# Performance work log

Measured on AMD Instinct MI355X. Metric: run time of the kernel, lower is better.

## Reference

```python
import jax, jax.numpy as jnp
import numpy as np

H = 8          # num_heads
EPS = 1e-5     # LayerNorm eps (torch default)


def _layernorm(x, gamma, beta):
    mu = jnp.mean(x, axis=-1, keepdims=True)
    var = jnp.mean(jnp.square(x - mu), axis=-1, keepdims=True)
    return (x - mu) * jax.lax.rsqrt(var + EPS) * gamma + beta


def setup_inputs() -> dict:
    key = jax.random.key(0)
    ks = jax.random.split(key, 20)
    B, S, D, F = 32, 1024, 256, 512
    d = D // H
    s = 1.0 / np.sqrt(D)
    sf = 1.0 / np.sqrt(F)
    inp = {
        "x": jax.random.normal(ks[0], (B, S, D), jnp.float32),
        "hidden": jax.random.normal(ks[1], (B, H, S, d), jnp.float32),
        # attention projections (torch Linear layout: [out, in])
        "Wq": jax.random.uniform(ks[2], (D, D), jnp.float32, -s, s),
        "bq": jnp.zeros((D,), jnp.float32),
        "Wk": jax.random.uniform(ks[3], (D, D), jnp.float32, -s, s),
        "bk": jnp.zeros((D,), jnp.float32),
        "Wv": jax.random.uniform(ks[4], (D, D), jnp.float32, -s, s),
        "bv": jnp.zeros((D,), jnp.float32),
        "Wo": jax.random.uniform(ks[5], (D, D), jnp.float32, -s, s),
        "bo": jnp.zeros((D,), jnp.float32),
        # layernorms
        "g1": jnp.ones((D,), jnp.float32),
        "be1": jnp.zeros((D,), jnp.float32),
        "g2": jnp.ones((D,), jnp.float32),
        "be2": jnp.zeros((D,), jnp.float32),
        # feed-forward
        "W1": jax.random.uniform(ks[6], (F, D), jnp.float32, -s, s),
        "b1": jnp.zeros((F,), jnp.float32),
        "W2": jax.random.uniform(ks[7], (D, F), jnp.float32, -sf, sf),
        "b2": jnp.zeros((D,), jnp.float32),
    }
    return inp


def reference(x, hidden, Wq, bq, Wk, bk, Wv, bv, Wo, bo, g1, be1, g2, be2, W1, b1, W2, b2):
    B, S, D = x.shape
    d = D // H
    scale = 1.0 / np.sqrt(d)

    def split_heads(t):  # [B,S,D] -> [B,H,S,d]
        return t.reshape(B, S, H, d).transpose(0, 2, 1, 3)

    q = split_heads(x @ Wq.T + bq)
    k = split_heads(x @ Wk.T + bk)
    v = split_heads(x @ Wv.T + bv)

    # scores with extra hidden-dependent bias: (q k^T + hidden k^T) / sqrt(d)
    scores = jnp.einsum("bhqd,bhkd->bhqk", q, k) * scale
    scores = scores + jnp.einsum("bhqd,bhkd->bhqk", hidden, k) * scale
    attn = jax.nn.softmax(scores, axis=-1)                 # [B,H,S,S]

    ctx = jnp.einsum("bhqk,bhkd->bhqd", attn, v)           # [B,H,S,d]
    ctx = ctx.transpose(0, 2, 1, 3).reshape(B, S, D)
    attn_out = ctx @ Wo.T + bo

    # x = x + x  (note: residual input discarded, attention output doubled)
    h = attn_out + attn_out
    # FFN with residual (dropout is identity at inference)
    h_norm = _layernorm(h, g1, be1)
    ff = jax.nn.relu(h_norm @ W1.T + b1) @ W2.T + b2
    h = h + ff
    # final: x = x + LayerNorm(x)
    h = h + _layernorm(h, g2, be2)
    return (h, attn)
```

## Files before the change

### kernel.cpp

```cpp
#include <hip/hip_runtime.h>

typedef __attribute__((ext_vector_type(8))) short short8;
typedef __attribute__((ext_vector_type(4))) float f32x4;

constexpr int NB  = 32;
constexpr int NS  = 1024;
constexpr int ND  = 256;
constexpr int NH  = 8;
constexpr int NDH = 32;
constexpr int NF  = 512;
constexpr int NM  = NB * NS;
#define RSD 0.17677669529663687f

static __device__ __forceinline__ ushort f2bf(float f) {
    union { float f; unsigned u; } v; v.f = f;
    unsigned r = v.u + 0x7fffu + ((v.u >> 16) & 1u);
    return (ushort)(r >> 16);
}
static __device__ __forceinline__ float bf2f(ushort u) {
    union { unsigned u; float f; } v; v.u = (unsigned)u << 16; return v.f;
}

__global__ __launch_bounds__(256) void split_hi(
    const float* __restrict__ in, ushort* __restrict__ hi, int n4)
{
    int i = blockIdx.x * 256 + threadIdx.x;
    if (i >= n4) return;
    float4 v = ((const float4*)in)[i];
    ushort4 h;
    h.x = f2bf(v.x); h.y = f2bf(v.y); h.z = f2bf(v.z); h.w = f2bf(v.w);
    ((ushort4*)hi)[i] = h;
}

__global__ __launch_bounds__(256) void split_weights(
    const float* __restrict__ Wq, const float* __restrict__ Wk,
    const float* __restrict__ Wv, const float* __restrict__ Wo,
    const float* __restrict__ W1, const float* __restrict__ W2,
    ushort* __restrict__ whi, ushort* __restrict__ wlo)
{
    const int seg = blockIdx.y;
    const float* src;
    size_t off;
    int n4;
    switch (seg) {
        case 0: src = Wq; off = 0;      n4 = 16384; break;
        case 1: src = Wk; off = 65536;  n4 = 16384; break;
        case 2: src = Wv; off = 131072; n4 = 16384; break;
        case 3: src = Wo; off = 196608; n4 = 16384; break;
        case 4: src = W1; off = 262144; n4 = 32768; break;
        default: src = W2; off = 393216; n4 = 32768; break;
    }
    int i = blockIdx.x * 256 + threadIdx.x;
    if (i >= n4) return;
    float4 v = ((const float4*)src)[i];
    ushort4 h, l;
    h.x = f2bf(v.x); l.x = f2bf(v.x - bf2f(h.x));
    h.y = f2bf(v.y); l.y = f2bf(v.y - bf2f(h.y));
    h.z = f2bf(v.z); l.z = f2bf(v.z - bf2f(h.z));
    h.w = f2bf(v.w); l.w = f2bf(v.w - bf2f(h.w));
    ((ushort4*)(whi + off))[i] = h;
    ((ushort4*)(wlo + off))[i] = l;
}

#define GEMM_CORE(K_, TERMS_)                                                  \
    __shared__ ushort sAh[128 * 40];                                           \
    __shared__ ushort sAl[(TERMS_ == 3) ? 128 * 40 : 8];                       \
    __shared__ ushort sBh[128 * 40], sBl[128 * 40];                            \
    const int t = threadIdx.x;                                                 \
    const int w = t >> 6, ln = t & 63;                                         \
    const int wr = w >> 1, wc = w & 1;                                         \
    const int col = ln & 15, quad = ln >> 4;                                   \
    const int srow = t >> 1, skb = (t & 1) << 4;                               \
    const ushort* gAh = Ahi + (size_t)(rbase + srow) * (K_) + skb;             \
    const ushort* gAl = (TERMS_ == 3) ? Alo + (size_t)(rbase + srow) * (K_) + skb : gAh; \
    const ushort* gBh = Whi + (size_t)(jbase + srow) * (K_) + skb;             \
    const ushort* gBl = Wlo + (size_t)(jbase + srow) * (K_) + skb;             \
    ushort* wAh = &sAh[srow * 40 + skb];                                       \
    ushort* wAl = (TERMS_ == 3) ? &sAl[srow * 40 + skb] : wAh;                 \
    ushort* wBh = &sBh[srow * 40 + skb];                                       \
    ushort* wBl = &sBl[srow * 40 + skb];                                       \
    f32x4 acc[4][4] = {};                                                      \
    short8 a0 = *(const short8*)(gAh);                                         \
    short8 a1 = *(const short8*)(gAh + 8);                                     \
    short8 c0 = {}, c1 = {};                                                   \
    if (TERMS_ == 3) { c0 = *(const short8*)(gAl); c1 = *(const short8*)(gAl + 8); } \
    short8 b0 = *(const short8*)(gBh);                                         \
    short8 b1 = *(const short8*)(gBh + 8);                                     \
    short8 d0 = *(const short8*)(gBl);                                         \
    short8 d1 = *(const short8*)(gBl + 8);                                     \
    for (int k0 = 0; k0 < (K_); k0 += 32) {                                    \
        __syncthreads();                                                       \
        *(short8*)wAh = a0; *(short8*)(wAh + 8) = a1;                          \
        if (TERMS_ == 3) { *(short8*)wAl = c0; *(short8*)(wAl + 8) = c1; }     \
        *(short8*)wBh = b0; *(short8*)(wBh + 8) = b1;                          \
        *(short8*)wBl = d0; *(short8*)(wBl + 8) = d1;                          \
        __syncthreads();                                                       \
        if (k0 + 32 < (K_)) {                                                  \
            a0 = *(const short8*)(gAh + k0 + 32);                              \
            a1 = *(const short8*)(gAh + k0 + 40);                              \
            if (TERMS_ == 3) {                                                 \
                c0 = *(const short8*)(gAl + k0 + 32);                          \
                c1 = *(const short8*)(gAl + k0 + 40);                          \
            }                                                                  \
            b0 = *(const short8*)(gBh + k0 + 32);                              \
            b1 = *(const short8*)(gBh + k0 + 40);                              \
            d0 = *(const short8*)(gBl + k0 + 32);                              \
            d1 = *(const short8*)(gBl + k0 + 40);                              \
        }                                                                      \
        short8 af[4], afl[4], bfv[4], bfl[4];                                  \
        _Pragma("unroll")                                                      \
        for (int m = 0; m < 4; ++m) {                                          \
            af[m]  = *(const short8*)&sAh[(wr * 64 + m * 16 + col) * 40 + quad * 8]; \
            if (TERMS_ == 3)                                                   \
                afl[m] = *(const short8*)&sAl[(wr * 64 + m * 16 + col) * 40 + quad * 8]; \
            bfv[m] = *(const short8*)&sBh[(wc * 64 + m * 16 + col) * 40 + quad * 8]; \
            bfl[m] = *(const short8*)&sBl[(wc * 64 + m * 16 + col) * 40 + quad * 8]; \
        }                                                                      \
        _Pragma("unroll")                                                      \
        for (int m = 0; m < 4; ++m)                                            \
            _Pragma("unroll")                                                  \
            for (int n = 0; n < 4; ++n) {                                      \
                acc[m][n] = __builtin_amdgcn_mfma_f32_16x16x32_bf16(af[m],  bfv[n], acc[m][n], 0, 0, 0); \
                acc[m][n] = __builtin_amdgcn_mfma_f32_16x16x32_bf16(af[m],  bfl[n], acc[m][n], 0, 0, 0); \
                if (TERMS_ == 3)                                               \
                    acc[m][n] = __builtin_amdgcn_mfma_f32_16x16x32_bf16(afl[m], bfv[n], acc[m][n], 0, 0, 0); \
            }                                                                  \
    }

template<int TERMS>
__global__ __launch_bounds__(256, TERMS == 2 ? 3 : 2) void gemm_mfma(
    const ushort* __restrict__ Ahi, const ushort* __restrict__ Alo,
    const ushort* __restrict__ Whi, const ushort* __restrict__ Wlo,
    const float* __restrict__ bias,
    float* __restrict__ outf, ushort* __restrict__ ohi,
    int N, int K, int epi)
{
    const int rbase = blockIdx.y << 7;
    const int jbase = blockIdx.x << 7;
    GEMM_CORE(K, TERMS)

    #pragma unroll
    for (int n = 0; n < 4; ++n) {
        const int cg = jbase + wc * 64 + n * 16 + col;
        const float bs = bias[cg];
        #pragma unroll
        for (int m = 0; m < 4; ++m) {
            #pragma unroll
            for (int r = 0; r < 4; ++r) {
                const int row = rbase + wr * 64 + m * 16 + quad * 4 + r;
                float v = acc[m][n][r] + bs;
                size_t oidx = (size_t)row * N + cg;
                if (epi == 0) {
                    outf[oidx] = 2.f * v;
                } else if (epi == 1) {
                    ohi[oidx] = f2bf(fmaxf(v, 0.f));
                } else {
                    outf[oidx] += v;
                }
            }
        }
    }
}

__global__ __launch_bounds__(256, 3) void gemm_qkv_mfma(
    const ushort* __restrict__ xhi,
    const ushort* __restrict__ whi, const ushort* __restrict__ wlo,
    const float* __restrict__ bq, const float* __restrict__ bk, const float* __restrict__ bv,
    const float* __restrict__ hidden,
    ushort* __restrict__ qhi, ushort* __restrict__ qlo,
    ushort* __restrict__ khi, ushort* __restrict__ klo,
    float* __restrict__ vb)
{
    const int z = blockIdx.z;
    const int rbase = blockIdx.y << 7;
    const int jbase = blockIdx.x << 7;
    const ushort* Ahi = xhi;
    const ushort* Alo = xhi;
    const ushort* Whi = whi + (size_t)z * 65536;
    const ushort* Wlo = wlo + (size_t)z * 65536;
    const float* bias = (z == 0) ? bq : (z == 1) ? bk : bv;
    GEMM_CORE(ND, 2)

    #pragma unroll
    for (int n = 0; n < 4; ++n) {
        const int cg = jbase + wc * 64 + n * 16 + col;
        const float bs = bias[cg];
        const int hh = cg >> 5, dd = cg & 31;
        #pragma unroll
        for (int m = 0; m < 4; ++m) {
            #pragma unroll
            for (int r = 0; r < 4; ++r) {
                const int row = rbase + wr * 64 + m * 16 + quad * 4 + r;
                const int b_i = row >> 10, s_i = row & 1023;
                size_t idx = (((size_t)(b_i * NH + hh)) * NS + s_i) * NDH + dd;
                float v = acc[m][n][r] + bs;
                if (z == 2) {
                    vb[idx] = v;
                } else if (z == 0) {
                    v = (v + hidden[idx]) * RSD;
                    ushort h = f2bf(v);
                    qhi[idx] = h;
                    qlo[idx] = f2bf(v - bf2f(h));
                } else {
                    ushort h = f2bf(v);
                    khi[idx] = h;
                    klo[idx] = f2bf(v - bf2f(h));
                }
            }
        }
    }
}

constexpr int VS  = 136;
constexpr int PST = 136;
__global__ __launch_bounds__(256, 4) void attn_flash(
    const ushort* __restrict__ qhi, const ushort* __restrict__ qlo,
    const ushort* __restrict__ khi, const ushort* __restrict__ klo,
    const float* __restrict__ vb,
    float* __restrict__ attn, ushort* __restrict__ cthi, ushort* __restrict__ ctlo)
{
    __shared__ ushort Vthi[32 * VS];
    __shared__ ushort Vtlo[32 * VS];
    __shared__ ushort Ps[4][16 * PST];
    const int bid = blockIdx.x;
    const int lid = (bid & 7) * 512 + (bid >> 3);
    const int qt = lid & 15, bh = lid >> 4;
    const int q0 = qt << 6;
    const int t = threadIdx.x;
    const int w = t >> 6, ln = t & 63;
    const int col = ln & 15, quad = ln >> 4;
    const int qr0 = q0 + 16 * w;
    ushort* myP = Ps[w];

    const size_t bhbase = (size_t)bh * NS * NDH;
    const size_t aoff = bhbase + (size_t)(qr0 + col) * NDH + quad * 8;
    const short8 ahi = *(const short8*)(qhi + aoff);
    const short8 alo = *(const short8*)(qlo + aoff);

    const float* vbase = vb + bhbase;
    const int sdd = t & 31, skg = (t >> 5) << 4;

    f32x4 acc0 = {0.f, 0.f, 0.f, 0.f}, acc1 = {0.f, 0.f, 0.f, 0.f};
    float S[4] = {0.f, 0.f, 0.f, 0.f};

    for (int k0 = 0; k0 < NS; k0 += 128) {
        __syncthreads();
        ushort hs[16], ls[16];
        #pragma unroll
        for (int c = 0; c < 16; ++c) {
            float xx = vbase[(size_t)(k0 + skg + c) * NDH + sdd];
            ushort h = f2bf(xx);
            hs[c] = h; ls[c] = f2bf(xx - bf2f(h));
        }
        #pragma unroll
        for (int c4 = 0; c4 < 4; ++c4) {
            ushort4 hv = make_ushort4(hs[c4 * 4], hs[c4 * 4 + 1], hs[c4 * 4 + 2], hs[c4 * 4 + 3]);
            ushort4 lv = make_ushort4(ls[c4 * 4], ls[c4 * 4 + 1], ls[c4 * 4 + 2], ls[c4 * 4 + 3]);
            *(ushort4*)&Vthi[sdd * VS + skg + c4 * 4] = hv;
            *(ushort4*)&Vtlo[sdd * VS + skg + c4 * 4] = lv;
        }
        __syncthreads();

        #pragma unroll
        for (int tl = 0; tl < 8; ++tl) {
            const int kk = k0 + tl * 16;
            const size_t boff = bhbase + (size_t)(kk + col) * NDH + quad * 8;
            short8 bhi = *(const short8*)(khi + boff);
            short8 blo = *(const short8*)(klo + boff);
            f32x4 c = {0.f, 0.f, 0.f, 0.f};
            c = __builtin_amdgcn_mfma_f32_16x16x32_bf16(ahi, bhi, c, 0, 0, 0);
            c = __builtin_amdgcn_mfma_f32_16x16x32_bf16(ahi, blo, c, 0, 0, 0);
            c = __builtin_amdgcn_mfma_f32_16x16x32_bf16(alo, bhi, c, 0, 0, 0);
            #pragma unroll
            for (int r = 0; r < 4; ++r) {
                float e = __expf(c[r]);
                S[r] += e;
                myP[(quad * 4 + r) * PST + tl * 16 + col] = f2bf(e);
            }
        }

        #pragma unroll
        for (int sl = 0; sl < 4; ++sl) {
            const int kl = sl * 32 + quad * 8;
            short8 pa = *(const short8*)&myP[col * PST + kl];
            short8 bhi0 = *(const short8*)&Vthi[col * VS + kl];
            short8 blo0 = *(const short8*)&Vtlo[col * VS + kl];
            short8 bhi1 = *(const short8*)&Vthi[(16 + col) * VS + kl];
            short8 blo1 = *(const short8*)&Vtlo[(16 + col) * VS + kl];
            acc0 = __builtin_amdgcn_mfma_f32_16x16x32_bf16(pa, bhi0, acc0, 0, 0, 0);
            acc0 = __builtin_amdgcn_mfma_f32_16x16x32_bf16(pa, blo0, acc0, 0, 0, 0);
            acc1 = __builtin_amdgcn_mfma_f32_16x16x32_bf16(pa, bhi1, acc1, 0, 0, 0);
            acc1 = __builtin_amdgcn_mfma_f32_16x16x32_bf16(pa, blo1, acc1, 0, 0, 0);
        }
    }

    float inv[4];
    #pragma unroll
    for (int r = 0; r < 4; ++r) {
        float s = S[r];
        #pragma unroll
        for (int m = 8; m >= 1; m >>= 1) s += __shfl_xor(s, m, 64);
        inv[r] = 1.f / s;
    }

    const int b_i = bh >> 3, hh = bh & 7;
    const int qrow = qr0 + quad * 4;
    #pragma unroll
    for (int r = 0; r < 4; ++r) {
        size_t base = ((size_t)b_i * NS + qrow + r) * ND + hh * NDH;
        float v0 = acc0[r] * inv[r], v1 = acc1[r] * inv[r];
        ushort h0 = f2bf(v0), h1 = f2bf(v1);
        cthi[base + col]      = h0;
        ctlo[base + col]      = f2bf(v0 - bf2f(h0));
        cthi[base + 16 + col] = h1;
        ctlo[base + 16 + col] = f2bf(v1 - bf2f(h1));
    }

    float* abase = attn + ((size_t)bh * NS + qrow) * NS;
    #pragma unroll 4
    for (int tl = 0; tl < 64; ++tl) {
        const int kk = tl * 16;
        const size_t boff = bhbase + (size_t)(kk + col) * NDH + quad * 8;
        short8 bhi = *(const short8*)(khi + boff);
        short8 blo = *(const short8*)(klo + boff);
        f32x4 c = {0.f, 0.f, 0.f, 0.f};
        c = __builtin_amdgcn_mfma_f32_16x16x32_bf16(ahi, bhi, c, 0, 0, 0);
        c = __builtin_amdgcn_mfma_f32_16x16x32_bf16(ahi, blo, c, 0, 0, 0);
        c = __builtin_amdgcn_mfma_f32_16x16x32_bf16(alo, bhi, c, 0, 0, 0);
        #pragma unroll
        for (int r = 0; r < 4; ++r) {
            float p = __expf(c[r]) * inv[r];
            __builtin_nontemporal_store(p, &abase[(size_t)r * NS + kk + col]);
        }
    }
}

__global__ __launch_bounds__(256) void ln_split(
    const float* __restrict__ x, const float* __restrict__ g,
    const float* __restrict__ be, ushort* __restrict__ ohi)
{
    const int t = threadIdx.x;
    const int wave = t >> 6, lane = t & 63;
    const int row = (blockIdx.x << 2) + wave;
    const float* xr = x + (size_t)row * ND;
    float4 v = *(const float4*)&xr[lane << 2];
    float s = v.x + v.y + v.z + v.w;
    #pragma unroll
    for (int m = 32; m >= 1; m >>= 1) s += __shfl_xor(s, m, 64);
    float mu = s * (1.f / 256.f);
    float dx = v.x - mu, dy = v.y - mu, dz = v.z - mu, dw = v.w - mu;
    float s2 = dx * dx + dy * dy + dz * dz + dw * dw;
    #pragma unroll
    for (int m = 32; m >= 1; m >>= 1) s2 += __shfl_xor(s2, m, 64);
    float rs = rsqrtf(s2 * (1.f / 256.f) + 1e-5f);
    float4 gv = *(const float4*)&g[lane << 2];
    float4 bv = *(const float4*)&be[lane << 2];
    ushort4 h;
    h.x = f2bf(dx * rs * gv.x + bv.x);
    h.y = f2bf(dy * rs * gv.y + bv.y);
    h.z = f2bf(dz * rs * gv.z + bv.z);
    h.w = f2bf(dw * rs * gv.w + bv.w);
    ((ushort4*)ohi)[((size_t)row * ND + (lane << 2)) >> 2] = h;
}

__global__ __launch_bounds__(256) void ln_final(
    const float* __restrict__ x, const float* __restrict__ g,
    const float* __restrict__ be, float* __restrict__ out)
{
    const int t = threadIdx.x;
    const int wave = t >> 6, lane = t & 63;
    const int row = (blockIdx.x << 2) + wave;
    const float* xr = x + (size_t)row * ND;
    float4 v = *(const float4*)&xr[lane << 2];
    float s = v.x + v.y + v.z + v.w;
    #pragma unroll
    for (int m = 32; m >= 1; m >>= 1) s += __shfl_xor(s, m, 64);
    float mu = s * (1.f / 256.f);
    float dx = v.x - mu, dy = v.y - mu, dz = v.z - mu, dw = v.w - mu;
    float s2 = dx * dx + dy * dy + dz * dz + dw * dw;
    #pragma unroll
    for (int m = 32; m >= 1; m >>= 1) s2 += __shfl_xor(s2, m, 64);
    float rs = rsqrtf(s2 * (1.f / 256.f) + 1e-5f);
    float4 gv = *(const float4*)&g[lane << 2];
    float4 bv = *(const float4*)&be[lane << 2];
    float4 o;
    o.x = dx * rs * gv.x + bv.x + v.x;
    o.y = dy * rs * gv.y + bv.y + v.y;
    o.z = dz * rs * gv.z + bv.z + v.z;
    o.w = dw * rs * gv.w + bv.w + v.w;
    *(float4*)&out[(size_t)row * ND + (lane << 2)] = o;
}

extern "C" void kernel_launch(void* const* d_in, const int* in_sizes, int n_in,
                              void* d_out, int out_size, void* d_ws, size_t ws_size,
                              hipStream_t stream)
{
    const float* x      = (const float*)d_in[0];
    const float* hidden = (const float*)d_in[1];
    const float* Wq = (const float*)d_in[2];
    const float* bq = (const float*)d_in[3];
    const float* Wk = (const float*)d_in[4];
    const float* bk = (const float*)d_in[5];
    const float* Wv = (const float*)d_in[6];
    const float* bv = (const float*)d_in[7];
    const float* Wo = (const float*)d_in[8];
    const float* bo = (const float*)d_in[9];
    const float* g1  = (const float*)d_in[10];
    const float* be1 = (const float*)d_in[11];
    const float* g2  = (const float*)d_in[12];
    const float* be2 = (const float*)d_in[13];
    const float* W1 = (const float*)d_in[14];
    const float* b1 = (const float*)d_in[15];
    const float* W2 = (const float*)d_in[16];
    const float* b2 = (const float*)d_in[17];

    float* out  = (float*)d_out;
    float* attn = out + (size_t)NM * ND;

    float* ws = (float*)d_ws;
    ushort* xhi  = (ushort*)ws;
    ushort* qhi  = (ushort*)(ws + 8388608);
    ushort* qlo  = (ushort*)(ws + 12582912);
    ushort* khi  = (ushort*)(ws + 16777216);
    ushort* klo  = (ushort*)(ws + 20971520);
    float*  vbuf = ws + 25165824;
    ushort* cthi = (ushort*)ws;
    ushort* ctlo = (ushort*)(ws + 4194304);
    float*  hbuf = ws + 33554432;
    ushort* hnhi = (ushort*)(ws + 8388608);
    ushort* ffhi = (ushort*)(ws + 16777216);
    ushort* whi  = (ushort*)(ws + 41943040);
    ushort* wlo  = (ushort*)(ws + 42205184);

    split_weights<<<dim3(128, 6), 256, 0, stream>>>(Wq, Wk, Wv, Wo, W1, W2, whi, wlo);
    split_hi<<<8192, 256, 0, stream>>>(x, xhi, 2097152);

    gemm_qkv_mfma<<<dim3(2, 256, 3), 256, 0, stream>>>(
        xhi, whi, wlo, bq, bk, bv, hidden, qhi, qlo, khi, klo, vbuf);
    attn_flash<<<dim3(4096), 256, 0, stream>>>(
        qhi, qlo, khi, klo, vbuf, attn, cthi, ctlo);
    gemm_mfma<3><<<dim3(2, 256), 256, 0, stream>>>(
        cthi, ctlo, whi + 196608, wlo + 196608, bo, hbuf, nullptr, ND, ND, 0);
    ln_split<<<NM / 4, 256, 0, stream>>>(hbuf, g1, be1, hnhi);
    gemm_mfma<2><<<dim3(4, 256), 256, 0, stream>>>(
        hnhi, nullptr, whi + 262144, wlo + 262144, b1, nullptr, ffhi, NF, ND, 1);
    gemm_mfma<2><<<dim3(2, 256), 256, 0, stream>>>(
        ffhi, nullptr, whi + 393216, wlo + 393216, b2, hbuf, nullptr, ND, NF, 2);
    ln_final<<<NM / 4, 256, 0, stream>>>(hbuf, g2, be2, out);
}
```

Before: 541.9 us.

## Load GEMM tiles straight to LDS with global_load_lds and XOR-swizzled layout

Replaces the register-staged global-to-LDS copy in the shared GEMM core with direct global_load_lds transfers. K-step tiles grow from 32 to 64 and use an XOR chunk swizzle instead of row padding to avoid bank conflicts. This removes the VGPR staging and the LDS store instructions and halves the number of barriers per K. In exchange it drops the software prefetch overlap, since loads are now issued and waited on between barriers. LDS use also roughly doubles, which may lower occupancy.

Measured after the change: 560.6 us. 3.5% more time.

```diff
diff --git a/kernel.cpp b/kernel.cpp
--- a/kernel.cpp
+++ b/kernel.cpp
@@ -19,6 +19,12 @@
 }
 static __device__ __forceinline__ float bf2f(ushort u) {
     union { unsigned u; float f; } v; v.u = (unsigned)u << 16; return v.f;
+}
+
+static __device__ __forceinline__ void gl16(const ushort* g, ushort* l) {
+    __builtin_amdgcn_global_load_lds(
+        (const __attribute__((address_space(1))) unsigned int*)(const void*)g,
+        (__attribute__((address_space(3))) unsigned int*)(void*)l, 16, 0, 0);
 }
 
 __global__ __launch_bounds__(256) void split_hi(
@@ -63,68 +69,60 @@
 }
 
 #define GEMM_CORE(K_, TERMS_)                                                  \
-    __shared__ ushort sAh[128 * 40];                                           \
-    __shared__ ushort sAl[(TERMS_ == 3) ? 128 * 40 : 8];                       \
-    __shared__ ushort sBh[128 * 40], sBl[128 * 40];                            \
+    __shared__ ushort sAh[128 * 64];                                           \
+    __shared__ ushort sAl[(TERMS_ == 3) ? 128 * 64 : 8];                       \
+    __shared__ ushort sBh[128 * 64];                                           \
+    __shared__ ushort sBl[128 * 64];                                           \
     const int t = threadIdx.x;                                                 \
     const int w = t >> 6, ln = t & 63;                                         \
     const int wr = w >> 1, wc = w & 1;                                         \
     const int col = ln & 15, quad = ln >> 4;                                   \
-    const int srow = t >> 1, skb = (t & 1) << 4;                               \
-    const ushort* gAh = Ahi + (size_t)(rbase + srow) * (K_) + skb;             \
-    const ushort* gAl = (TERMS_ == 3) ? Alo + (size_t)(rbase + srow) * (K_) + skb : gAh; \
-    const ushort* gBh = Whi + (size_t)(jbase + srow) * (K_) + skb;             \
-    const ushort* gBl = Wlo + (size_t)(jbase + srow) * (K_) + skb;             \
-    ushort* wAh = &sAh[srow * 40 + skb];                                       \
-    ushort* wAl = (TERMS_ == 3) ? &sAl[srow * 40 + skb] : wAh;                 \
-    ushort* wBh = &sBh[srow * 40 + skb];                                       \
-    ushort* wBl = &sBl[srow * 40 + skb];                                       \
+    const int srow8 = ln >> 3;                                                 \
+    const int schk  = ln & 7;                                                  \
     f32x4 acc[4][4] = {};                                                      \
-    short8 a0 = *(const short8*)(gAh);                                         \
-    short8 a1 = *(const short8*)(gAh + 8);                                     \
-    short8 c0 = {}, c1 = {};                                                   \
-    if (TERMS_ == 3) { c0 = *(const short8*)(gAl); c1 = *(const short8*)(gAl + 8); } \
-    short8 b0 = *(const short8*)(gBh);                                         \
-    short8 b1 = *(const short8*)(gBh + 8);                                     \
-    short8 d0 = *(const short8*)(gBl);                                         \
-    short8 d1 = *(const short8*)(gBl + 8);                                     \
-    for (int k0 = 0; k0 < (K_); k0 += 32) {                                    \
+    for (int k0 = 0; k0 < (K_); k0 += 64) {                                    \
         __syncthreads();                                                       \
-        *(short8*)wAh = a0; *(short8*)(wAh + 8) = a1;                          \
-        if (TERMS_ == 3) { *(short8*)wAl = c0; *(short8*)(wAl + 8) = c1; }     \
-        *(short8*)wBh = b0; *(short8*)(wBh + 8) = b1;                          \
-        *(short8*)wBl = d0; *(short8*)(wBl + 8) = d1;                          \
+        _Pragma("unroll")                                                      \
+        for (int i = 0; i < 4; ++i) {                                          \
+            const int blk = w * 4 + i;                                         \
+            const int row = blk * 8 + srow8;                                   \
+            const int chunk = schk ^ (row & 7);                                \
+            gl16(Ahi + (size_t)(rbase + row) * (K_) + k0 + chunk * 8,          \
+                 &sAh[blk * 512]);                                             \
+            if (TERMS_ == 3)                                                   \
+                gl16(Alo + (size_t)(rbase + row) * (K_) + k0 + chunk * 8,      \
+                     &sAl[blk * 512]);                                         \
+            gl16(Whi + (size_t)(jbase + row) * (K_) + k0 + chunk * 8,          \
+                 &sBh[blk * 512]);                                             \
+            gl16(Wlo + (size_t)(jbase + row) * (K_) + k0 + chunk * 8,          \
+                 &sBl[blk * 512]);                                             \
+        }                                                                      \
         __syncthreads();                                                       \
-        if (k0 + 32 < (K_)) {                                                  \
-            a0 = *(const short8*)(gAh + k0 + 32);                              \
-            a1 = *(const short8*)(gAh + k0 + 40);                              \
-            if (TERMS_ == 3) {                                                 \
-                c0 = *(const short8*)(gAl + k0 + 32);                          \
-                c1 = *(const short8*)(gAl + k0 + 40);                          \
+        _Pragma("unroll")                                                      \
+        for (int ks = 0; ks < 2; ++ks) {                                       \
+            short8 af[4], afl[4], bfv[4], bfl[4];                              \
+            const int kc = ks * 4 + quad;                                      \
+            _Pragma("unroll")                                                  \
+            for (int m = 0; m < 4; ++m) {                                      \
+                const int ra = wr * 64 + m * 16 + col;                         \
+                const int rb = wc * 64 + m * 16 + col;                         \
+                const int oa = ra * 64 + ((kc ^ (ra & 7)) << 3);               \
+                const int ob = rb * 64 + ((kc ^ (rb & 7)) << 3);               \
+                af[m]  = *(const short8*)&sAh[oa];                             \
+                if (TERMS_ == 3) afl[m] = *(const short8*)&sAl[oa];            \
+                bfv[m] = *(const short8*)&sBh[ob];                             \
+                bfl[m] = *(const short8*)&sBl[ob];                             \
             }                                                                  \
-            b0 = *(const short8*)(gBh + k0 + 32);                              \
-            b1 = *(const short8*)(gBh + k0 + 40);                              \
-            d0 = *(const short8*)(gBl + k0 + 32);                              \
-            d1 = *(const short8*)(gBl + k0 + 40);                              \
+            _Pragma("unroll")                                                  \
+            for (int m = 0; m < 4; ++m)                                        \
+                _Pragma("unroll")                                              \
+                for (int n = 0; n < 4; ++n) {                                  \
+                    acc[m][n] = __builtin_amdgcn_mfma_f32_16x16x32_bf16(af[m],  bfv[n], acc[m][n], 0, 0, 0); \
+                    acc[m][n] = __builtin_amdgcn_mfma_f32_16x16x32_bf16(af[m],  bfl[n], acc[m][n], 0, 0, 0); \
+                    if (TERMS_ == 3)                                           \
+                        acc[m][n] = __builtin_amdgcn_mfma_f32_16x16x32_bf16(afl[m], bfv[n], acc[m][n], 0, 0, 0); \
+                }                                                              \
         }                                                                      \
-        short8 af[4], afl[4], bfv[4], bfl[4];                                  \
-        _Pragma("unroll")                                                      \
-        for (int m = 0; m < 4; ++m) {                                          \
-            af[m]  = *(const short8*)&sAh[(wr * 64 + m * 16 + col) * 40 + quad * 8]; \
-            if (TERMS_ == 3)                                                   \
-                afl[m] = *(const short8*)&sAl[(wr * 64 + m * 16 + col) * 40 + quad * 8]; \
-            bfv[m] = *(const short8*)&sBh[(wc * 64 + m * 16 + col) * 40 + quad * 8]; \
-            bfl[m] = *(const short8*)&sBl[(wc * 64 + m * 16 + col) * 40 + quad * 8]; \
-        }                                                                      \
-        _Pragma("unroll")                                                      \
-        for (int m = 0; m < 4; ++m)                                            \
-            _Pragma("unroll")                                                  \
-            for (int n = 0; n < 4; ++n) {                                      \
-                acc[m][n] = __builtin_amdgcn_mfma_f32_16x16x32_bf16(af[m],  bfv[n], acc[m][n], 0, 0, 0); \
-                acc[m][n] = __builtin_amdgcn_mfma_f32_16x16x32_bf16(af[m],  bfl[n], acc[m][n], 0, 0, 0); \
-                if (TERMS_ == 3)                                               \
-                    acc[m][n] = __builtin_amdgcn_mfma_f32_16x16x32_bf16(afl[m], bfv[n], acc[m][n], 0, 0, 0); \
-            }                                                                  \
     }
 
 template<int TERMS>
```
